# Optimization experiments

Measured on AMD Instinct MI355X. Metric: run time of the kernel, lower is better.

Reference implementation:

```python
import jax, jax.numpy as jnp
import numpy as np

N_EMBD = 512
Q_N_EMBD = 512
N_HEAD = 8
EPS = 1e-5


def _layernorm(x, w, b):
    mu = jnp.mean(x, axis=-1, keepdims=True)
    var = jnp.mean(jnp.square(x - mu), axis=-1, keepdims=True)
    return (x - mu) * jax.lax.rsqrt(var + EPS) * w + b


def setup_inputs() -> dict:
    key = jax.random.key(0)
    ks = jax.random.split(key, 16)
    B, C, H, W = 8, N_EMBD, 32, 32
    s = 1.0 / np.sqrt(N_EMBD)
    inp = {
        "q": jax.random.normal(ks[0], (B, Q_N_EMBD, H, W), jnp.float32),
        "kv": jax.random.normal(ks[1], (B, C, H, W), jnp.float32),
        "ln_kv_w": jnp.ones((N_EMBD,), jnp.float32),
        "ln_kv_b": jnp.zeros((N_EMBD,), jnp.float32),
        "ln_q_w": jnp.ones((Q_N_EMBD,), jnp.float32),
        "ln_q_b": jnp.zeros((Q_N_EMBD,), jnp.float32),
        "Wk": jax.random.normal(ks[2], (N_EMBD, N_EMBD), jnp.float32) * s,
        "bk": jnp.zeros((N_EMBD,), jnp.float32),
        "Wq": jax.random.normal(ks[3], (Q_N_EMBD, N_EMBD), jnp.float32) * s,
        "bq": jnp.zeros((N_EMBD,), jnp.float32),
        "Wv": jax.random.normal(ks[4], (N_EMBD, N_EMBD), jnp.float32) * s,
        "bv": jnp.zeros((N_EMBD,), jnp.float32),
        "Wp": jax.random.normal(ks[5], (N_EMBD, N_EMBD), jnp.float32) * s,
        "bp": jnp.zeros((N_EMBD,), jnp.float32),
    }
    return inp


def reference(q, kv, ln_kv_w, ln_kv_b, ln_q_w, ln_q_b,
              Wk, bk, Wq, bq, Wv, bv, Wp, bp):
    B, C, H, W = kv.shape
    c_q = q.shape[1]
    T = H * W
    hd = C // N_HEAD  # head dim

    # [B, C, H, W] -> [B, T, C] tokens
    kv_t = kv.reshape(B, C, T).transpose(0, 2, 1)
    q_t = q.reshape(B, c_q, T).transpose(0, 2, 1)

    kv_n = _layernorm(kv_t, ln_kv_w, ln_kv_b)
    q_n = _layernorm(q_t, ln_q_w, ln_q_b)

    # projections, split heads: [B, T, C] -> [B, H, T, hd]
    def heads(x):
        return x.reshape(B, T, N_HEAD, hd).transpose(0, 2, 1, 3)

    k = heads(kv_n @ Wk + bk)
    qh = heads(q_n @ Wq + bq)
    v = heads(kv_n @ Wv + bv)

    att = jnp.einsum('bhqd,bhkd->bhqk', qh, k) * (1.0 / np.sqrt(hd))
    att = jax.nn.softmax(att, axis=-1)
    y = jnp.einsum('bhqk,bhkd->bhqd', att, v)
    y = y.transpose(0, 2, 1, 3).reshape(B, T, C)
    y = y @ Wp + bp

    x = kv_t + y  # residual on (pre-LN) kv tokens
    return x.transpose(0, 2, 1).reshape(B, C, H, W)
```

## Files before the change

kernel.cpp:

```cpp
#include <hip/hip_runtime.h>
#include <stdint.h>

#define DI static __device__ __forceinline__

typedef __attribute__((ext_vector_type(8))) short bh8;
typedef __attribute__((ext_vector_type(4))) float f4;
typedef __attribute__((ext_vector_type(4))) unsigned int u4;

DI short f2bf(float f) {
  unsigned u = __float_as_uint(f);
  u += 0x7fffu + ((u >> 16) & 1u);
  return (short)(u >> 16);
}

DI unsigned pkbf(float a, float b) {
  unsigned ua = __float_as_uint(a) + 0x8000u;
  unsigned ub = __float_as_uint(b) + 0x8000u;
  return __builtin_amdgcn_perm(ub, ua, 0x07060302u);
}

DI void gll16(const void* g, void* l) {
  __builtin_amdgcn_global_load_lds(
      (const __attribute__((address_space(1))) unsigned int*)g,
      (__attribute__((address_space(3))) unsigned int*)l, 16, 0, 0);
}

DI f4 mfma16(bh8 a, bh8 b, f4 c) {
  return __builtin_amdgcn_mfma_f32_16x16x32_bf16(a, b, c, 0, 0, 0);
}

DI f4 mfma8(long a, long b, f4 c) {
  return __builtin_amdgcn_mfma_f32_16x16x32_fp8_fp8(a, b, c, 0, 0, 0);
}

DI bh8 ld8(const short* p) { return *(const bh8*)p; }

DI float bf2f(short s) {
  return __uint_as_float(((unsigned)(unsigned short)s) << 16);
}

DI long cvt8(bh8 v) {
  int lo = 0, hi = 0;
  lo = __builtin_amdgcn_cvt_pk_fp8_f32(bf2f(v[0]), bf2f(v[1]), lo, false);
  lo = __builtin_amdgcn_cvt_pk_fp8_f32(bf2f(v[2]), bf2f(v[3]), lo, true);
  hi = __builtin_amdgcn_cvt_pk_fp8_f32(bf2f(v[4]), bf2f(v[5]), hi, false);
  hi = __builtin_amdgcn_cvt_pk_fp8_f32(bf2f(v[6]), bf2f(v[7]), hi, true);
  return ((long)(unsigned)lo) | ((long)hi << 32);
}

__global__ __launch_bounds__(256) void prep_k(
    const float* __restrict__ kv, const float* __restrict__ qi,
    const float* __restrict__ kw, const float* __restrict__ kbv,
    const float* __restrict__ qw, const float* __restrict__ qbv,
    const float* __restrict__ Wk, const float* __restrict__ Wq,
    const float* __restrict__ Wv, const float* __restrict__ Wp,
    short* __restrict__ kvn, short* __restrict__ qn,
    short* __restrict__ Wt)
{
  __shared__ char sm[16 * 516 * 4 + 128];
  int role = blockIdx.y;
  int bx = blockIdx.x;
  int tid = threadIdx.x;

  if (role < 4) {
    if (bx >= 256) return;
    float (*ts)[33] = (float(*)[33])sm;
    const float* w = (role == 0) ? Wk : (role == 1) ? Wq : (role == 2) ? Wv : Wp;
    short* o = Wt + ((size_t)role << 18);
    int c0 = (bx & 15) << 5, r0 = (bx >> 4) << 5;
    int tx = tid & 31, ty = tid >> 5;
#pragma unroll
    for (int k = 0; k < 32; k += 8)
      ts[ty + k][tx] = w[((size_t)(r0 + ty + k) << 9) + c0 + tx];
    __syncthreads();
#pragma unroll
    for (int k = 0; k < 32; k += 8)
      o[((size_t)(c0 + ty + k) << 9) + r0 + tx] = f2bf(ts[tx][ty + k]);
    return;
  }

  float (*xs)[516] = (float(*)[516])sm;
  float* smean = (float*)(sm + 16 * 516 * 4);
  float* srstd = smean + 16;
  int which = role - 4;
  const float* x = which ? qi : kv;
  const float* w = which ? qw : kw;
  const float* bb = which ? qbv : kbv;
  short* o = which ? qn : kvn;
  int b = bx >> 6;
  int t0 = (bx & 63) << 4;
  const float* xb = x + ((size_t)b << 19) + (size_t)t0;
#pragma unroll
  for (int k = 0; k < 8; k++) {
    int idx = (k << 8) + tid;
    int c = idx >> 2, tt = (idx & 3) << 2;
    float4 v = *(const float4*)(xb + ((size_t)c << 10) + tt);
    xs[tt + 0][c] = v.x; xs[tt + 1][c] = v.y;
    xs[tt + 2][c] = v.z; xs[tt + 3][c] = v.w;
  }
  __syncthreads();
  {
    int t = tid >> 4, cp = tid & 15;
    float s = 0.f, s2 = 0.f;
#pragma unroll
    for (int k = 0; k < 8; k++) {
      float4 v = *(const float4*)&xs[t][(cp << 2) + (k << 6)];
      s  += v.x + v.y + v.z + v.w;
      s2 += v.x * v.x + v.y * v.y + v.z * v.z + v.w * v.w;
    }
#pragma unroll
    for (int m = 1; m < 16; m <<= 1) {
      s  += __shfl_xor(s,  m);
      s2 += __shfl_xor(s2, m);
    }
    if (cp == 0) {
      float mean = s * (1.f / 512.f);
      float var  = s2 * (1.f / 512.f) - mean * mean;
      smean[t] = mean;
      srstd[t] = rsqrtf(var + 1e-5f);
    }
  }
  __syncthreads();
#pragma unroll
  for (int k = 0; k < 8; k++) {
    int idx = (k << 8) + tid;
    int t = idx >> 7, c = (idx & 127) << 2;
    float4 v = *(const float4*)&xs[t][c];
    float4 wv = *(const float4*)(w + c);
    float4 bv4 = *(const float4*)(bb + c);
    float mu = smean[t], rs = srstd[t];
    float r0 = (v.x - mu) * rs * wv.x + bv4.x;
    float r1 = (v.y - mu) * rs * wv.y + bv4.y;
    float r2 = (v.z - mu) * rs * wv.z + bv4.z;
    float r3 = (v.w - mu) * rs * wv.w + bv4.w;
    uint2 pk; pk.x = pkbf(r0, r1); pk.y = pkbf(r2, r3);
    *(uint2*)(o + (((size_t)(b << 10) + t0 + t) << 9) + c) = pk;
  }
}

__global__ __launch_bounds__(256, 3) void gemm_qkv_k(
    const short* __restrict__ kvn, const short* __restrict__ qn,
    const short* __restrict__ Wt,
    const float* __restrict__ bk, const float* __restrict__ bq,
    const float* __restrict__ bv,
    short* __restrict__ kbuf, short* __restrict__ qbuf,
    short* __restrict__ vtb)
{
  __shared__ short As[128 * 64];
  __shared__ short Bs[128 * 64];
  int z = blockIdx.z;
  const short* A; const short* Bt; const float* bias; short* outp;
  int m0, n0;
  if (z == 0)      { A = kvn;            Bt = Wt;             bias = bk; outp = kbuf; }
  else if (z == 1) { A = qn;             Bt = Wt + (1 << 18); bias = bq; outp = qbuf; }
  else             { A = Wt + (2 << 18); Bt = kvn;            bias = bv; outp = vtb; }
  if (z == 2) { m0 = blockIdx.y << 7; n0 = blockIdx.x << 7; }
  else        { m0 = blockIdx.x << 7; n0 = blockIdx.y << 7; }
  int tid = threadIdx.x;
  int lane = tid & 63, wid = tid >> 6;
  int r = lane & 15, g = lane >> 4;
  int wrow = (wid >> 1) << 6, wcol = (wid & 1) << 6;
  f4 acc[4][4];
#pragma unroll
  for (int i = 0; i < 4; i++)
#pragma unroll
    for (int j = 0; j < 4; j++) {
      acc[i][j][0] = 0.f; acc[i][j][1] = 0.f;
      acc[i][j][2] = 0.f; acc[i][j][3] = 0.f;
    }
  for (int k0 = 0; k0 < 512; k0 += 64) {
    __syncthreads();
#pragma unroll
    for (int it = 0; it < 4; it++) {
      int n = (it << 8) + tid;
      int row = n >> 3;
      int c = (n & 7) ^ (row & 7);
      gll16(A  + ((size_t)(m0 + row) << 9) + k0 + (c << 3), As + (n << 3));
      gll16(Bt + ((size_t)(n0 + row) << 9) + k0 + (c << 3), Bs + (n << 3));
    }
    __syncthreads();
    bh8 a[2][4], b[2][4];
#pragma unroll
    for (int ks = 0; ks < 2; ks++) {
#pragma unroll
      for (int i = 0; i < 4; i++) {
        int R = wrow + (i << 4) + r;
        a[ks][i] = ld8(As + (R << 6) + ((((ks << 2) + g) ^ (R & 7)) << 3));
      }
#pragma unroll
      for (int j = 0; j < 4; j++) {
        int R = wcol + (j << 4) + r;
        b[ks][j] = ld8(Bs + (R << 6) + ((((ks << 2) + g) ^ (R & 7)) << 3));
      }
    }
#pragma unroll
    for (int ks = 0; ks < 2; ks++)
#pragma unroll
      for (int i = 0; i < 4; i++)
#pragma unroll
        for (int j = 0; j < 4; j++)
          acc[i][j] = mfma16(a[ks][i], b[ks][j], acc[i][j]);
  }
#pragma unroll
  for (int i = 0; i < 4; i++) {
#pragma unroll
    for (int j = 0; j < 4; j++) {
      int mm = m0 + wrow + (i << 4) + (g << 2);
      int nn = n0 + wcol + (j << 4) + r;
      if (z != 2) {
        float bvv = bias[nn];
        int h = nn >> 6, d = nn & 63;
#pragma unroll
        for (int q = 0; q < 4; q++) {
          int m = mm + q;
          int bb = m >> 10, t = m & 1023;
          outp[((((size_t)(bb * 8 + h)) << 10) + t) * 64 + d] =
              f2bf(acc[i][j][q] + bvv);
        }
      } else {
        int bb = nn >> 10, t = nn & 1023;
#pragma unroll
        for (int q = 0; q < 4; q++) {
          int m = mm + q;
          int h = m >> 6, d = m & 63;
          outp[((((size_t)(bb * 8 + h)) << 6) + d) * 1024 + t] =
              f2bf(acc[i][j][q] + bias[m]);
        }
      }
    }
  }
}

__global__ __launch_bounds__(256, 2) void gemm_proj_k(
    const short* __restrict__ A, const short* __restrict__ Bt,
    const float* __restrict__ bias, float* __restrict__ outp,
    const float* __restrict__ resid)
{
  __shared__ short As[64 * 64];
  __shared__ short Bs[128 * 64];
  int m0 = blockIdx.y << 6, n0 = blockIdx.x << 7;
  int tid = threadIdx.x;
  int lane = tid & 63, wid = tid >> 6;
  int r = lane & 15, g = lane >> 4;
  int wrow = (wid >> 1) << 5, wcol = (wid & 1) << 6;
  f4 acc[2][4];
#pragma unroll
  for (int i = 0; i < 2; i++)
#pragma unroll
    for (int j = 0; j < 4; j++) {
      acc[i][j][0] = 0.f; acc[i][j][1] = 0.f;
      acc[i][j][2] = 0.f; acc[i][j][3] = 0.f;
    }
  for (int k0 = 0; k0 < 512; k0 += 64) {
    __syncthreads();
#pragma unroll
    for (int it = 0; it < 2; it++) {
      int n = (it << 8) + tid;
      int row = n >> 3;
      int c = (n & 7) ^ (row & 7);
      gll16(A + ((size_t)(m0 + row) << 9) + k0 + (c << 3), As + (n << 3));
    }
#pragma unroll
    for (int it = 0; it < 4; it++) {
      int n = (it << 8) + tid;
      int row = n >> 3;
      int c = (n & 7) ^ (row & 7);
      gll16(Bt + ((size_t)(n0 + row) << 9) + k0 + (c << 3), Bs + (n << 3));
    }
    __syncthreads();
    bh8 a[2][2], b[2][4];
#pragma unroll
    for (int ks = 0; ks < 2; ks++) {
#pragma unroll
      for (int i = 0; i < 2; i++) {
        int R = wrow + (i << 4) + r;
        a[ks][i] = ld8(As + (R << 6) + ((((ks << 2) + g) ^ (R & 7)) << 3));
      }
#pragma unroll
      for (int j = 0; j < 4; j++) {
        int R = wcol + (j << 4) + r;
        b[ks][j] = ld8(Bs + (R << 6) + ((((ks << 2) + g) ^ (R & 7)) << 3));
      }
    }
#pragma unroll
    for (int ks = 0; ks < 2; ks++)
#pragma unroll
      for (int i = 0; i < 2; i++)
#pragma unroll
        for (int j = 0; j < 4; j++)
          acc[i][j] = mfma16(a[ks][i], b[ks][j], acc[i][j]);
  }
#pragma unroll
  for (int i = 0; i < 2; i++) {
#pragma unroll
    for (int j = 0; j < 4; j++) {
      int mm = m0 + wrow + (i << 4) + (g << 2);
      int nn = n0 + wcol + (j << 4) + r;
      int bb = nn >> 10, t = nn & 1023;
#pragma unroll
      for (int q = 0; q < 4; q++) {
        int m = mm + q;
        size_t ad = ((((size_t)bb << 9) + m) << 10) + t;
        outp[ad] = acc[i][j][q] + bias[m] + resid[ad];
      }
    }
  }
}

__global__ __launch_bounds__(256, 2) void attn_k(
    const short* __restrict__ qb, const short* __restrict__ kb,
    const short* __restrict__ vtb, short* __restrict__ yo)
{
  __shared__ char Ks[256 * 64];
  __shared__ char Vs[64 * 256];
  __shared__ char Ps[128 * 256];
  int h = blockIdx.x, b = blockIdx.z;
  int qt0 = blockIdx.y << 7;
  int tid = threadIdx.x, lane = tid & 63, wid = tid >> 6;
  int r = lane & 15, g = lane >> 4;
  int wbase = wid << 5;
  size_t bh = (size_t)(b * 8 + h);
  const short* Qg = qb  + ((bh << 10) + qt0) * 64;
  const short* Kg = kb  + (bh << 10) * 64;
  const short* Vg = vtb + (bh << 6) * 1024;

  long qf8[2][2];
#pragma unroll
  for (int i = 0; i < 2; i++)
#pragma unroll
    for (int ksd = 0; ksd < 2; ksd++)
      qf8[i][ksd] = cvt8(ld8(Qg + ((size_t)(wbase + (i << 4) + r) << 6) +
                             (ksd << 5) + (g << 3)));

  const long ONES = 0x3838383838383838L;

  f4 oac[2][4], sacc[2];
#pragma unroll
  for (int i = 0; i < 2; i++) {
#pragma unroll
    for (int jn = 0; jn < 4; jn++) {
      oac[i][jn][0] = 0.f; oac[i][jn][1] = 0.f;
      oac[i][jn][2] = 0.f; oac[i][jn][3] = 0.f;
    }
    sacc[i][0] = 0.f; sacc[i][1] = 0.f; sacc[i][2] = 0.f; sacc[i][3] = 0.f;
  }

  const float csc = 0.18033688011112042f;

  for (int ck = 0; ck < 4; ck++) {
    __syncthreads();
    {
      const short* Kc = Kg + ((size_t)(ck << 8) << 6);
#pragma unroll
      for (int it = 0; it < 8; it++) {
        int c = (it << 5) + (tid >> 3);
        int db = tid & 7;
        bh8 kv8 = ld8(Kc + ((size_t)c << 6) + (db << 3));
        int p = ((c & 15) << 4) | (c >> 4);
        *(long*)(Ks + (p << 6) + ((db ^ (p & 7)) << 3)) = cvt8(kv8);
      }
      const short* Vc = Vg + (ck << 8);
#pragma unroll
      for (int it = 0; it < 8; it++) {
        int d = (it << 3) + (tid >> 5);
        int tb = tid & 31;
        bh8 vv8 = ld8(Vc + ((size_t)d << 10) + (tb << 3));
        *(long*)(Vs + (d << 8) + ((tb ^ (d & 31)) << 3)) = cvt8(vv8);
      }
    }
    __syncthreads();

    long kf[2][16];
    f4 s[16];
#pragma unroll
    for (int i = 0; i < 2; i++) {
#pragma unroll
      for (int j = 0; j < 16; j++) {
        s[j][0] = 0.f; s[j][1] = 0.f; s[j][2] = 0.f; s[j][3] = 0.f;
      }
#pragma unroll
      for (int ksd = 0; ksd < 2; ksd++)
#pragma unroll
        for (int j = 0; j < 16; j++) {
          if (i == 0)
            kf[ksd][j] = *(const long*)(Ks + (((j << 4) + r) << 6) +
                            ((((ksd << 2) + g) ^ (r & 7)) << 3));
          s[j] = mfma8(qf8[i][ksd], kf[ksd][j], s[j]);
        }
#pragma unroll
      for (int q = 0; q < 4; q++) {
        float e[16];
#pragma unroll
        for (int j = 0; j < 16; j++)
          e[j] = __builtin_amdgcn_exp2f(
                     fminf(fmaf(s[j][q], csc, -3.0f), 8.5f));
        int w0 = 0, w1 = 0, w2 = 0, w3 = 0;
        w0 = __builtin_amdgcn_cvt_pk_fp8_f32(e[0],  e[1],  w0, false);
        w0 = __builtin_amdgcn_cvt_pk_fp8_f32(e[2],  e[3],  w0, true);
        w1 = __builtin_amdgcn_cvt_pk_fp8_f32(e[4],  e[5],  w1, false);
        w1 = __builtin_amdgcn_cvt_pk_fp8_f32(e[6],  e[7],  w1, true);
        w2 = __builtin_amdgcn_cvt_pk_fp8_f32(e[8],  e[9],  w2, false);
        w2 = __builtin_amdgcn_cvt_pk_fp8_f32(e[10], e[11], w2, true);
        w3 = __builtin_amdgcn_cvt_pk_fp8_f32(e[12], e[13], w3, false);
        w3 = __builtin_amdgcn_cvt_pk_fp8_f32(e[14], e[15], w3, true);
        long plo = ((long)(unsigned)w0) | ((long)w1 << 32);
        long phi = ((long)(unsigned)w2) | ((long)w3 << 32);
        int row = wbase + (i << 4) + (g << 2) + q;
        int cc = r ^ (row & 15);
        *(long*)(Ps + (row << 8) + (cc << 4))     = plo;
        *(long*)(Ps + (row << 8) + (cc << 4) + 8) = phi;
      }
    }

#pragma unroll
    for (int ks = 0; ks < 8; ks++) {
      long ap[2];
#pragma unroll
      for (int i = 0; i < 2; i++) {
        int row = wbase + (i << 4) + r;
        int cc = ((ks << 1) + (g >> 1)) ^ (row & 15);
        ap[i] = *(const long*)(Ps + (row << 8) + (cc << 4) + ((g & 1) << 3));
        sacc[i] = mfma8(ap[i], ONES, sacc[i]);
      }
#pragma unroll
      for (int jn = 0; jn < 4; jn++) {
        int d = (jn << 4) + r;
        long bv8 = *(const long*)(Vs + (d << 8) +
                      ((((ks << 2) + g) ^ (d & 31)) << 3));
#pragma unroll
        for (int i = 0; i < 2; i++)
          oac[i][jn] = mfma8(ap[i], bv8, oac[i][jn]);
      }
    }
  }

#pragma unroll
  for (int i = 0; i < 2; i++)
#pragma unroll
    for (int q = 0; q < 4; q++) {
      float inv = 1.f / (sacc[i][q] + 1e-20f);
      int trow = qt0 + wbase + (i << 4) + (g << 2) + q;
      size_t base = (((size_t)(b << 10) + trow) << 9) + (h << 6);
#pragma unroll
      for (int jn = 0; jn < 4; jn++)
        yo[base + (jn << 4) + r] = f2bf(oac[i][jn][q] * inv);
    }
}

extern "C" void kernel_launch(void* const* d_in, const int* in_sizes, int n_in,
                              void* d_out, int out_size, void* d_ws, size_t ws_size,
                              hipStream_t stream)
{
  const float* q    = (const float*)d_in[0];
  const float* kv   = (const float*)d_in[1];
  const float* lnkw = (const float*)d_in[2];
  const float* lnkb = (const float*)d_in[3];
  const float* lnqw = (const float*)d_in[4];
  const float* lnqb = (const float*)d_in[5];
  const float* Wk   = (const float*)d_in[6];
  const float* bk   = (const float*)d_in[7];
  const float* Wq   = (const float*)d_in[8];
  const float* bq   = (const float*)d_in[9];
  const float* Wv   = (const float*)d_in[10];
  const float* bv   = (const float*)d_in[11];
  const float* Wp   = (const float*)d_in[12];
  const float* bp   = (const float*)d_in[13];

  char* ws = (char*)d_ws;
  const size_t SZ = (size_t)8192 * 512 * 2;
  short* buf0 = (short*)(ws);
  short* qn   = (short*)(ws + SZ);
  short* kbuf = (short*)(ws + 2 * SZ);
  short* qbuf = (short*)(ws + 3 * SZ);
  short* vtb  = (short*)(ws + 4 * SZ);
  short* Wt   = (short*)(ws + 5 * SZ);
  if (ws_size < 5 * SZ + 4 * 512 * 512 * 2) return;

  prep_k<<<dim3(512, 6), 256, 0, stream>>>(kv, q, lnkw, lnkb, lnqw, lnqb,
                                           Wk, Wq, Wv, Wp, buf0, qn, Wt);
  gemm_qkv_k<<<dim3(64, 4, 3), 256, 0, stream>>>(buf0, qn, Wt, bk, bq, bv,
                                                 kbuf, qbuf, vtb);
  attn_k<<<dim3(8, 8, 8), 256, 0, stream>>>(qbuf, kbuf, vtb, buf0);
  gemm_proj_k<<<dim3(64, 8), 256, 0, stream>>>(Wt + (3 << 18), buf0, bp,
                                               (float*)d_out, kv);
}
```

Baseline: 183.4 us.

## Emit FP8 Q/K/V in attention-ready swizzled layout from QKV GEMM

The QKV projection epilogue now converts outputs directly to fp8 and writes K and V in the exact swizzled, chunked shared-memory layout the attention kernel expects. The attention kernel can then stage K/V tiles with direct global-to-LDS 16-byte loads instead of loading bf16, converting and scattering. This halves intermediate traffic and removes conversion work from attention. The cost is byte-granular scattered stores in the GEMM epilogue, which may coalesce poorly.

```diff
diff --git a/kernel.cpp b/kernel.cpp
--- a/kernel.cpp
+++ b/kernel.cpp
@@ -5,7 +5,6 @@
 
 typedef __attribute__((ext_vector_type(8))) short bh8;
 typedef __attribute__((ext_vector_type(4))) float f4;
-typedef __attribute__((ext_vector_type(4))) unsigned int u4;
 
 DI short f2bf(float f) {
   unsigned u = __float_as_uint(f);
@@ -19,6 +18,10 @@
   return __builtin_amdgcn_perm(ub, ua, 0x07060302u);
 }
 
+DI unsigned char f2fp8(float f) {
+  return (unsigned char)(__builtin_amdgcn_cvt_pk_fp8_f32(f, f, 0, false) & 0xff);
+}
+
 DI void gll16(const void* g, void* l) {
   __builtin_amdgcn_global_load_lds(
       (const __attribute__((address_space(1))) unsigned int*)g,
@@ -34,19 +37,6 @@
 }
 
 DI bh8 ld8(const short* p) { return *(const bh8*)p; }
-
-DI float bf2f(short s) {
-  return __uint_as_float(((unsigned)(unsigned short)s) << 16);
-}
-
-DI long cvt8(bh8 v) {
-  int lo = 0, hi = 0;
-  lo = __builtin_amdgcn_cvt_pk_fp8_f32(bf2f(v[0]), bf2f(v[1]), lo, false);
-  lo = __builtin_amdgcn_cvt_pk_fp8_f32(bf2f(v[2]), bf2f(v[3]), lo, true);
-  hi = __builtin_amdgcn_cvt_pk_fp8_f32(bf2f(v[4]), bf2f(v[5]), hi, false);
-  hi = __builtin_amdgcn_cvt_pk_fp8_f32(bf2f(v[6]), bf2f(v[7]), hi, true);
-  return ((long)(unsigned)lo) | ((long)hi << 32);
-}
 
 __global__ __launch_bounds__(256) void prep_k(
     const float* __restrict__ kv, const float* __restrict__ qi,
@@ -143,17 +133,17 @@
     const short* __restrict__ Wt,
     const float* __restrict__ bk, const float* __restrict__ bq,
     const float* __restrict__ bv,
-    short* __restrict__ kbuf, short* __restrict__ qbuf,
-    short* __restrict__ vtb)
+    unsigned char* __restrict__ kb8, unsigned char* __restrict__ qb8,
+    unsigned char* __restrict__ vb8)
 {
   __shared__ short As[128 * 64];
   __shared__ short Bs[128 * 64];
   int z = blockIdx.z;
-  const short* A; const short* Bt; const float* bias; short* outp;
+  const short* A; const short* Bt; const float* bias;
   int m0, n0;
-  if (z == 0)      { A = kvn;            Bt = Wt;             bias = bk; outp = kbuf; }
-  else if (z == 1) { A = qn;             Bt = Wt + (1 << 18); bias = bq; outp = qbuf; }
-  else             { A = Wt + (2 << 18); Bt = kvn;            bias = bv; outp = vtb; }
+  if (z == 0)      { A = kvn;            Bt = Wt;             bias = bk; }
+  else if (z == 1) { A = qn;             Bt = Wt + (1 << 18); bias = bq; }
+  else             { A = Wt + (2 << 18); Bt = kvn;            bias = bv; }
   if (z == 2) { m0 = blockIdx.y << 7; n0 = blockIdx.x << 7; }
   else        { m0 = blockIdx.x << 7; n0 = blockIdx.y << 7; }
   int tid = threadIdx.x;
@@ -207,24 +197,39 @@
     for (int j = 0; j < 4; j++) {
       int mm = m0 + wrow + (i << 4) + (g << 2);
       int nn = n0 + wcol + (j << 4) + r;
-      if (z != 2) {
+      if (z == 0) {
         float bvv = bias[nn];
         int h = nn >> 6, d = nn & 63;
 #pragma unroll
         for (int q = 0; q < 4; q++) {
           int m = mm + q;
           int bb = m >> 10, t = m & 1023;
-          outp[((((size_t)(bb * 8 + h)) << 10) + t) * 64 + d] =
-              f2bf(acc[i][j][q] + bvv);
+          int c = t & 255;
+          int p = ((c & 15) << 4) | (c >> 4);
+          size_t base = ((size_t)((bb * 8 + h) * 4 + (t >> 8)) << 14);
+          kb8[base + (p << 6) + (((d >> 3) ^ (p & 7)) << 3) + (d & 7)] =
+              f2fp8(acc[i][j][q] + bvv);
+        }
+      } else if (z == 1) {
+        float bvv = bias[nn];
+        int h = nn >> 6, d = nn & 63;
+#pragma unroll
+        for (int q = 0; q < 4; q++) {
+          int m = mm + q;
+          int bb = m >> 10, t = m & 1023;
+          qb8[((((size_t)(bb * 8 + h)) << 10) + t) * 64 + d] =
+              f2fp8(acc[i][j][q] + bvv);
         }
       } else {
         int bb = nn >> 10, t = nn & 1023;
+        int tb = (t & 255) >> 3;
 #pragma unroll
         for (int q = 0; q < 4; q++) {
           int m = mm + q;
           int h = m >> 6, d = m & 63;
-          outp[((((size_t)(bb * 8 + h)) << 6) + d) * 1024 + t] =
-              f2bf(acc[i][j][q] + bias[m]);
+          size_t base = ((size_t)((bb * 8 + h) * 4 + (t >> 8)) << 14);
+          vb8[base + (d << 8) + ((tb ^ (d & 31)) << 3) + (t & 7)] =
+              f2fp8(acc[i][j][q] + bias[m]);
         }
       }
     }
@@ -308,29 +313,29 @@
 }
 
 __global__ __launch_bounds__(256, 2) void attn_k(
-    const short* __restrict__ qb, const short* __restrict__ kb,
-    const short* __restrict__ vtb, short* __restrict__ yo)
+    const unsigned char* __restrict__ qb8, const unsigned char* __restrict__ kb8,
+    const unsigned char* __restrict__ vb8, short* __restrict__ yo)
 {
-  __shared__ char Ks[256 * 64];
-  __shared__ char Vs[64 * 256];
-  __shared__ char Ps[128 * 256];
+  __shared__ char Ks[16384];
+  __shared__ char Vs[16384];
+  __shared__ char Ps[32768];
   int h = blockIdx.x, b = blockIdx.z;
   int qt0 = blockIdx.y << 7;
   int tid = threadIdx.x, lane = tid & 63, wid = tid >> 6;
   int r = lane & 15, g = lane >> 4;
   int wbase = wid << 5;
   size_t bh = (size_t)(b * 8 + h);
-  const short* Qg = qb  + ((bh << 10) + qt0) * 64;
-  const short* Kg = kb  + (bh << 10) * 64;
-  const short* Vg = vtb + (bh << 6) * 1024;
+  const unsigned char* Qg = qb8 + ((bh << 10) + qt0) * 64;
+  const unsigned char* Kg = kb8 + (bh << 16);
+  const unsigned char* Vg = vb8 + (bh << 16);
 
   long qf8[2][2];
 #pragma unroll
   for (int i = 0; i < 2; i++)
 #pragma unroll
     for (int ksd = 0; ksd < 2; ksd++)
-      qf8[i][ksd] = cvt8(ld8(Qg + ((size_t)(wbase + (i << 4) + r) << 6) +
-                             (ksd << 5) + (g << 3)));
+      qf8[i][ksd] = *(const long*)(Qg +
+          ((size_t)(wbase + (i << 4) + r) << 6) + (((ksd << 2) + g) << 3));
 
   const long ONES = 0x3838383838383838L;
 
@@ -349,24 +354,11 @@
 
   for (int ck = 0; ck < 4; ck++) {
     __syncthreads();
-    {
-      const short* Kc = Kg + ((size_t)(ck << 8) << 6);
-#pragma unroll
-      for (int it = 0; it < 8; it++) {
-        int c = (it << 5) + (tid >> 3);
-        int db = tid & 7;
-        bh8 kv8 = ld8(Kc + ((size_t)c << 6) + (db << 3));
-        int p = ((c & 15) << 4) | (c >> 4);
-        *(long*)(Ks + (p << 6) + ((db ^ (p & 7)) << 3)) = cvt8(kv8);
-      }
-      const short* Vc = Vg + (ck << 8);
-#pragma unroll
-      for (int it = 0; it < 8; it++) {
-        int d = (it << 3) + (tid >> 5);
-        int tb = tid & 31;
-        bh8 vv8 = ld8(Vc + ((size_t)d << 10) + (tb << 3));
-        *(long*)(Vs + (d << 8) + ((tb ^ (d & 31)) << 3)) = cvt8(vv8);
-      }
+#pragma unroll
+    for (int it = 0; it < 4; it++) {
+      int n = ((it << 8) + tid) << 4;
+      gll16(Kg + (ck << 14) + n, Ks + n);
+      gll16(Vg + (ck << 14) + n, Vs + n);
     }
     __syncthreads();
 
@@ -470,17 +462,17 @@
   const size_t SZ = (size_t)8192 * 512 * 2;
   short* buf0 = (short*)(ws);
   short* qn   = (short*)(ws + SZ);
-  short* kbuf = (short*)(ws + 2 * SZ);
-  short* qbuf = (short*)(ws + 3 * SZ);
-  short* vtb  = (short*)(ws + 4 * SZ);
+  unsigned char* kb8 = (unsigned char*)(ws + 2 * SZ);
+  unsigned char* qb8 = (unsigned char*)(ws + 3 * SZ);
+  unsigned char* vb8 = (unsigned char*)(ws + 4 * SZ);
   short* Wt   = (short*)(ws + 5 * SZ);
   if (ws_size < 5 * SZ + 4 * 512 * 512 * 2) return;
 
   prep_k<<<dim3(512, 6), 256, 0, stream>>>(kv, q, lnkw, lnkb, lnqw, lnqb,
                                            Wk, Wq, Wv, Wp, buf0, qn, Wt);
   gemm_qkv_k<<<dim3(64, 4, 3), 256, 0, stream>>>(buf0, qn, Wt, bk, bq, bv,
-                                                 kbuf, qbuf, vtb);
-  attn_k<<<dim3(8, 8, 8), 256, 0, stream>>>(qbuf, kbuf, vtb, buf0);
+                                                 kb8, qb8, vb8);
+  attn_k<<<dim3(8, 8, 8), 256, 0, stream>>>(qb8, kb8, vb8, buf0);
   gemm_proj_k<<<dim3(64, 8), 256, 0, stream>>>(Wt + (3 << 18), buf0, bp,
                                                (float*)d_out, kv);
 }
```

Result: faster. 169.8 us (-7.4%).
